# Optimization experiments

Measured on AMD Instinct MI355X. Metric: run time of the kernel, lower is better.

Reference implementation:

```python
import jax, jax.numpy as jnp
import numpy as np

N = 50000
E = 800000
H, C = 8, 16          # heads, per-head channels (H*C = 128)
G = 64                # number of graphs
EPS = 1e-5


def setup_inputs() -> dict:
    key = jax.random.key(0)
    ks = jax.random.split(key, 8)
    x = jax.random.normal(ks[0], (N, 128), dtype=jnp.float32)
    edge_index = jax.random.randint(ks[1], (2, E), 0, N, dtype=jnp.int64)
    batch = jnp.sort(jax.random.randint(ks[2], (N,), 0, G, dtype=jnp.int64))
    W = jax.random.normal(ks[3], (3, 128, 128), dtype=jnp.float32) * 0.08
    att_src = jax.random.normal(ks[4], (3, H, C), dtype=jnp.float32) * 0.1
    att_dst = jax.random.normal(ks[5], (3, H, C), dtype=jnp.float32) * 0.1
    bias = jnp.zeros((3, 128), dtype=jnp.float32)
    gamma = jnp.ones((3, 128), dtype=jnp.float32)
    beta = jnp.zeros((3, 128), dtype=jnp.float32)
    ro_w = jax.random.normal(ks[6], (128, 2), dtype=jnp.float32) * 0.08
    ro_b = jnp.zeros((2,), dtype=jnp.float32)
    return {"x": x, "edge_index": edge_index, "batch": batch, "W": W,
            "att_src": att_src, "att_dst": att_dst, "bias": bias,
            "gamma": gamma, "beta": beta, "ro_w": ro_w, "ro_b": ro_b}


def _gat_block(prev, h, src, dst, W, a_s, a_d, b, g, be):
    # GATConv (concat=True, add_self_loops already applied to src/dst)
    xp = (h @ W).reshape(N, H, C)                       # [N,H,C]
    al_s = jnp.sum(xp * a_s, axis=-1)                   # [N,H]
    al_d = jnp.sum(xp * a_d, axis=-1)                   # [N,H]
    logits = jax.nn.leaky_relu(al_s[src] + al_d[dst], negative_slope=0.2)  # [Et,H]
    m = jax.ops.segment_max(logits, dst, num_segments=N)        # softmax over dst groups
    ex = jnp.exp(logits - m[dst])
    denom = jax.ops.segment_sum(ex, dst, num_segments=N)
    alpha = ex / denom[dst]                              # [Et,H]
    msg = xp[src] * alpha[:, :, None]                    # [Et,H,C]
    agg = jax.ops.segment_sum(msg, dst, num_segments=N).reshape(N, H * C) + b
    y = prev + agg
    # BatchNorm1d (training mode: batch stats, biased variance)
    mu = y.mean(axis=0)
    var = y.var(axis=0)
    yn = (y - mu) / jnp.sqrt(var + EPS) * g + be
    return jax.nn.elu(yn)


def reference(x, edge_index, batch, W, att_src, att_dst, bias, gamma, beta, ro_w, ro_b):
    loops = jnp.arange(N, dtype=edge_index.dtype)
    src = jnp.concatenate([edge_index[0], loops])        # PyG add_self_loops=True
    dst = jnp.concatenate([edge_index[1], loops])
    h = x
    prev = jnp.zeros((N, 128), dtype=x.dtype)
    for i in range(3):
        out = _gat_block(prev, h, src, dst, W[i], att_src[i], att_dst[i],
                         bias[i], gamma[i], beta[i])
        prev = h[:, :128]
        h = out
    # global mean pool over graphs
    sums = jax.ops.segment_sum(h, batch, num_segments=G)
    cnt = jax.ops.segment_sum(jnp.ones((N,), dtype=h.dtype), batch, num_segments=G)
    pooled = sums / jnp.maximum(cnt, 1.0)[:, None]
    return pooled @ ro_w + ro_b
```

## Files before the change

### kernel.cpp

```cpp
#include <hip/hip_runtime.h>
#include <hip/hip_bf16.h>
#include <math.h>

#define NN 50000
#define EE 800000
#define MM (EE + NN)
#define GG 64
#define SWG 512
#define NSB ((NN + 255) / 256)
#define PSP 16

__device__ __forceinline__ int geti(const void* p, long idx, int is64) {
    return is64 ? (int)((const long long*)p)[idx] : ((const int*)p)[idx];
}

__device__ __forceinline__ float bf2f(unsigned short u) {
    return __uint_as_float(((unsigned)u) << 16);
}

__device__ __forceinline__ float eluf(float z) {
    return z > 0.f ? z : expm1f(z);
}

__global__ void k_detect(const int* __restrict__ ei, int* __restrict__ flag) {
    if (blockIdx.x == 0 && threadIdx.x == 0) {
        int ok = 1;
        for (int k = 0; k < 128; ++k) {
            int lo = ei[2 * k], hi = ei[2 * k + 1];
            if (hi != 0 || (unsigned)lo >= (unsigned)NN) { ok = 0; break; }
        }
        flag[0] = ok;
    }
}


__global__ void k_zero(int* p, int n) {
    int i = blockIdx.x * blockDim.x + threadIdx.x;
    if (i < n) p[i] = 0;
}

__global__ void k_count(const void* __restrict__ ei, const int* __restrict__ flag,
                        int* __restrict__ counts) {
    int e = blockIdx.x * blockDim.x + threadIdx.x;
    if (e >= MM) return;
    int is64 = flag[0];
    int d = (e < EE) ? geti(ei, (long)EE + e, is64) : (e - EE);
    if ((unsigned)d < (unsigned)NN) atomicAdd(&counts[d], 1);
}

__global__ __launch_bounds__(256) void k_scan1(const int* __restrict__ counts,
                                               int* __restrict__ rowptr,
                                               int* __restrict__ bsum) {
    __shared__ int buf[256];
    int b = blockIdx.x, tid = threadIdx.x;
    int i = b * 256 + tid;
    int v = (i < NN) ? counts[i] : 0;
    buf[tid] = v;
    __syncthreads();
    for (int off = 1; off < 256; off <<= 1) {
        int t = (tid >= off) ? buf[tid - off] : 0;
        __syncthreads();
        buf[tid] += t;
        __syncthreads();
    }
    if (i < NN) rowptr[i + 1] = buf[tid];
    if (tid == 255) bsum[b] = buf[255];
}

__global__ __launch_bounds__(256) void k_scan2(int* __restrict__ bsum) {
    __shared__ int buf[256];
    int tid = threadIdx.x;
    int v = (tid < NSB) ? bsum[tid] : 0;
    buf[tid] = v;
    __syncthreads();
    for (int off = 1; off < 256; off <<= 1) {
        int t = (tid >= off) ? buf[tid - off] : 0;
        __syncthreads();
        buf[tid] += t;
        __syncthreads();
    }
    if (tid < NSB) bsum[tid] = (tid == 0) ? 0 : buf[tid - 1];
}

__global__ __launch_bounds__(256) void k_scan3(int* __restrict__ rowptr,
                                               const int* __restrict__ bsum) {
    int b = blockIdx.x, tid = threadIdx.x;
    int i = b * 256 + tid;
    if (i < NN) rowptr[i + 1] += bsum[b];
    if (b == 0 && tid == 0) rowptr[0] = 0;
}

__global__ void k_fill(const void* __restrict__ ei, const int* __restrict__ flag,
                       const int* __restrict__ rowptr,
                       int* __restrict__ fill, int* __restrict__ colv) {
    int e = blockIdx.x * blockDim.x + threadIdx.x;
    if (e >= MM) return;
    int is64 = flag[0];
    int s, d;
    if (e < EE) { s = geti(ei, e, is64); d = geti(ei, (long)EE + e, is64); }
    else { s = d = e - EE; }
    if ((unsigned)d >= (unsigned)NN || (unsigned)s >= (unsigned)NN) return;
    int pos = rowptr[d] + atomicAdd(&fill[d], 1);
    if ((unsigned)pos < (unsigned)MM) colv[pos] = s;
}


__global__ __launch_bounds__(256) void k_gemm_att(
    const float* __restrict__ hsrc, const float* __restrict__ Ysrc,
    const float* __restrict__ st, const float* __restrict__ W,
    const float* __restrict__ attS, const float* __restrict__ attD,
    unsigned short* __restrict__ xpb, float* __restrict__ als,
    float* __restrict__ ald, int n)
{
    __shared__ float Wt[32][128];
    __shared__ float Ht[128][33];
    int tid = threadIdx.x;
    int head = tid & 7, r0 = tid >> 3;
    int rbase = blockIdx.x * 128;
    bool useY = (Ysrc != nullptr);

    float acc[4][16];
#pragma unroll
    for (int a = 0; a < 4; ++a)
#pragma unroll
        for (int b = 0; b < 16; ++b) acc[a][b] = 0.f;

    for (int k0 = 0; k0 < 128; k0 += 32) {
#pragma unroll
        for (int j = 0; j < 4; ++j) {
            int idx = tid * 16 + j * 4;
            int kk = idx >> 7, c = idx & 127;
            *(float4*)&Wt[kk][c] = *(const float4*)&W[(k0 + kk) * 128 + c];
        }
#pragma unroll
        for (int j = 0; j < 4; ++j) {
            int f = tid * 16 + j * 4;
            int r = f >> 5, kk = f & 31;
            int gr = rbase + r;
            float4 v = make_float4(0.f, 0.f, 0.f, 0.f);
            if (gr < n) {
                if (useY) {
                    float4 yv = *(const float4*)&Ysrc[gr * 128 + k0 + kk];
                    float4 scv = *(const float4*)&st[k0 + kk];
                    float4 shv = *(const float4*)&st[128 + k0 + kk];
                    v.x = eluf(fmaf(yv.x, scv.x, shv.x));
                    v.y = eluf(fmaf(yv.y, scv.y, shv.y));
                    v.z = eluf(fmaf(yv.z, scv.z, shv.z));
                    v.w = eluf(fmaf(yv.w, scv.w, shv.w));
                } else {
                    v = *(const float4*)&hsrc[gr * 128 + k0 + kk];
                }
            }
            Ht[r][kk] = v.x; Ht[r][kk + 1] = v.y; Ht[r][kk + 2] = v.z; Ht[r][kk + 3] = v.w;
        }
        __syncthreads();
#pragma unroll
        for (int kk = 0; kk < 32; ++kk) {
            float wv[16];
#pragma unroll
            for (int j = 0; j < 4; ++j)
                *(float4*)&wv[j * 4] = *(const float4*)&Wt[kk][head * 16 + j * 4];
#pragma unroll
            for (int rr = 0; rr < 4; ++rr) {
                float hv = Ht[r0 + rr * 32][kk];
#pragma unroll
                for (int j = 0; j < 16; ++j) acc[rr][j] = fmaf(hv, wv[j], acc[rr][j]);
            }
        }
        __syncthreads();
    }

    float asv[16], adv[16];
#pragma unroll
    for (int j = 0; j < 16; ++j) { asv[j] = attS[head * 16 + j]; adv[j] = attD[head * 16 + j]; }

#pragma unroll
    for (int rr = 0; rr < 4; ++rr) {
        int r = rbase + r0 + rr * 32;
        if (r < n) {
            float ds = 0.f, dd = 0.f;
#pragma unroll
            for (int j = 0; j < 16; ++j) { ds = fmaf(acc[rr][j], asv[j], ds); dd = fmaf(acc[rr][j], adv[j], dd); }
            als[r * 8 + head] = ds;
            ald[r * 8 + head] = dd;
            unsigned short xb[16];
#pragma unroll
            for (int j = 0; j < 16; ++j) {
                __hip_bfloat16 t = __float2bfloat16(acc[rr][j]);
                xb[j] = *reinterpret_cast<unsigned short*>(&t);
            }
            *(uint4*)&xpb[r * 128 + head * 16]     = *(uint4*)&xb[0];
            *(uint4*)&xpb[r * 128 + head * 16 + 8] = *(uint4*)&xb[8];
        }
    }
}


__global__ __launch_bounds__(256) void k_agg(
    const unsigned short* __restrict__ xpb, const float* __restrict__ als,
    const float* __restrict__ ald,
    const int* __restrict__ rowptr, const int* __restrict__ colv,
    const float* __restrict__ prevRaw, const float* __restrict__ prevY,
    const float* __restrict__ pst, const float* __restrict__ bias,
    float* __restrict__ y, int n)
{
    __shared__ float alds[4][8][8];
    __shared__ int   slds[4][8];
    int wv = threadIdx.x >> 6;
    int wid = (int)((blockIdx.x * blockDim.x + threadIdx.x) >> 6);
    int lane = threadIdx.x & 63;
    if (wid >= n) return;
    int rs = rowptr[wid], re = rowptr[wid + 1];
    int deg = re - rs;

    int hd = lane & 7;
    int ee = lane >> 3;
    float aldn = ald[wid * 8 + hd];
    int q = lane >> 3;
    int c0 = lane * 2;

    float a0 = 0.f, a1 = 0.f, smloc = 0.f;
    int full = deg & ~7;

    for (int b0 = 0; b0 < full; b0 += 8) {
        int se = colv[rs + b0 + ee];
        float v = als[se * 8 + hd] + aldn;
        v = v > 0.f ? v : 0.2f * v;
        float al = expf(v);
        smloc += al;
        alds[wv][ee][hd] = al;
        if (hd == 0) slds[wv][ee] = se;
#pragma unroll
        for (int j = 0; j < 8; ++j) {
            int s = slds[wv][j];
            float a = alds[wv][j][q];
            ushort2 xv = *(const ushort2*)(xpb + (size_t)s * 128 + c0);
            a0 = fmaf(a, bf2f(xv.x), a0);
            a1 = fmaf(a, bf2f(xv.y), a1);
        }
    }

    if (full < deg) {
        int nb = deg - full;
        float al = 0.f;
        int se = 0;
        if (ee < nb) {
            se = colv[rs + full + ee];
            float v = als[se * 8 + hd] + aldn;
            v = v > 0.f ? v : 0.2f * v;
            al = expf(v);
            smloc += al;
        }
        alds[wv][ee][hd] = al;
        if (hd == 0) slds[wv][ee] = se;
        for (int j = 0; j < nb; ++j) {
            int s = slds[wv][j];
            float a = alds[wv][j][q];
            ushort2 xv = *(const ushort2*)(xpb + (size_t)s * 128 + c0);
            a0 = fmaf(a, bf2f(xv.x), a0);
            a1 = fmaf(a, bf2f(xv.y), a1);
        }
    }

    smloc += __shfl_xor(smloc, 8);
    smloc += __shfl_xor(smloc, 16);
    smloc += __shfl_xor(smloc, 32);
    float inv = 1.f / __shfl(smloc, q);
    a0 *= inv;
    a1 *= inv;

    float p0 = 0.f, p1 = 0.f;
    if (prevY) {
        float2 yv = *(const float2*)(prevY + (size_t)wid * 128 + c0);
        p0 = eluf(fmaf(yv.x, pst[c0], pst[128 + c0]));
        p1 = eluf(fmaf(yv.y, pst[c0 + 1], pst[129 + c0]));
    } else if (prevRaw) {
        p0 = prevRaw[(size_t)wid * 128 + c0];
        p1 = prevRaw[(size_t)wid * 128 + c0 + 1];
    }
    y[wid * 128 + c0] = p0 + a0 + bias[c0];
    y[wid * 128 + c0 + 1] = p1 + a1 + bias[c0 + 1];
}


__global__ __launch_bounds__(256) void k_stats(const float* __restrict__ y,
                                               double* __restrict__ partial, int n) {
    int col = threadIdx.x & 127;
    int rg = threadIdx.x >> 7;
    double s = 0.0, s2 = 0.0;
    for (int r = blockIdx.x * 2 + rg; r < n; r += SWG * 2) {
        float v = y[r * 128 + col];
        s += v; s2 += (double)v * (double)v;
    }
    __shared__ double ls[256], ls2[256];
    ls[threadIdx.x] = s; ls2[threadIdx.x] = s2;
    __syncthreads();
    if (rg == 0) {
        s += ls[threadIdx.x + 128];
        s2 += ls2[threadIdx.x + 128];
        partial[col * SWG + blockIdx.x] = s;
        partial[128 * SWG + col * SWG + blockIdx.x] = s2;
    }
}

__global__ void k_stats_fin(const double* __restrict__ partial,
                            const float* __restrict__ gamma,
                            const float* __restrict__ beta,
                            float* __restrict__ st, int n) {
    int col = threadIdx.x;
    double s = 0.0, s2 = 0.0;
    for (int w = 0; w < SWG; ++w) {
        s += partial[col * SWG + w];
        s2 += partial[128 * SWG + col * SWG + w];
    }
    double mu = s / n;
    double var = s2 / n - mu * mu;
    double rsig = 1.0 / sqrt(var + 1e-5);
    double sc = (double)gamma[col] * rsig;
    st[col] = (float)sc;
    st[128 + col] = (float)((double)beta[col] - mu * sc);
}


__global__ __launch_bounds__(256) void k_pool_part(
    const float* __restrict__ Y, const float* __restrict__ st,
    const void* __restrict__ batch, const int* __restrict__ flag,
    float* __restrict__ ppart, int n)
{
    int g = blockIdx.x / PSP;
    int sp = blockIdx.x % PSP;
    int is64 = flag[0];
    int lo = 0, hi = n;
    while (lo < hi) { int mid = (lo + hi) >> 1; if (geti(batch, mid, is64) < g) lo = mid + 1; else hi = mid; }
    int start = lo;
    hi = n;
    while (lo < hi) { int mid = (lo + hi) >> 1; if (geti(batch, mid, is64) < g + 1) lo = mid + 1; else hi = mid; }
    int end = lo;
    int cnt = end - start;
    int slice = (cnt + PSP - 1) / PSP;
    int s0 = start + sp * slice;
    int s1 = s0 + slice; if (s1 > end) s1 = end;

    int col = threadIdx.x & 127;
    int half = threadIdx.x >> 7;
    float sc = st[col], sh = st[128 + col];
    float s = 0.f;
    for (int r = s0 + half; r < s1; r += 2)
        s += eluf(fmaf(Y[(size_t)r * 128 + col], sc, sh));
    __shared__ float ls[256];
    ls[threadIdx.x] = s;
    __syncthreads();
    if (half == 0) ppart[(g * PSP + sp) * 128 + col] = s + ls[col + 128];
}

__global__ __launch_bounds__(128) void k_pool_fin(
    const float* __restrict__ ppart, const void* __restrict__ batch,
    const int* __restrict__ flag, const float* __restrict__ row,
    const float* __restrict__ rob, float* __restrict__ out, int n)
{
    int g = blockIdx.x;
    int is64 = flag[0];
    int lo = 0, hi = n;
    while (lo < hi) { int mid = (lo + hi) >> 1; if (geti(batch, mid, is64) < g) lo = mid + 1; else hi = mid; }
    int start = lo;
    hi = n;
    while (lo < hi) { int mid = (lo + hi) >> 1; if (geti(batch, mid, is64) < g + 1) lo = mid + 1; else hi = mid; }
    int cnt = lo - start;

    int col = threadIdx.x;
    float s = 0.f;
#pragma unroll
    for (int sp = 0; sp < PSP; ++sp) s += ppart[(g * PSP + sp) * 128 + col];
    __shared__ float ls[128];
    ls[col] = s * (1.f / fmaxf((float)cnt, 1.f));
    __syncthreads();
    if (col < 2) {
        float acc = 0.f;
        for (int c = 0; c < 128; ++c) acc = fmaf(ls[c], row[c * 2 + col], acc);
        out[g * 2 + col] = acc + rob[col];
    }
}


extern "C" void kernel_launch(void* const* d_in, const int* in_sizes, int n_in,
                              void* d_out, int out_size, void* d_ws, size_t ws_size,
                              hipStream_t stream) {
    const float* x     = (const float*)d_in[0];
    const void*  ei    = d_in[1];
    const void*  batch = d_in[2];
    const float* W     = (const float*)d_in[3];
    const float* attS  = (const float*)d_in[4];
    const float* attD  = (const float*)d_in[5];
    const float* bias  = (const float*)d_in[6];
    const float* gamma = (const float*)d_in[7];
    const float* beta  = (const float*)d_in[8];
    const float* row   = (const float*)d_in[9];
    const float* rob   = (const float*)d_in[10];
    float* out = (float*)d_out;

    char* wsb = (char*)d_ws;
    size_t off = 0;
    auto alloc = [&](size_t bytes) {
        void* p = wsb + off;
        off += (bytes + 255) & ~(size_t)255;
        return p;
    };
    int*    flag    = (int*)alloc(256);
    int*    rowptr  = (int*)alloc((size_t)(NN + 1) * 4);
    int*    cnts    = (int*)alloc((size_t)NN * 4 * 2);
    int*    bsum    = (int*)alloc((size_t)256 * 4);
    int*    colv    = (int*)alloc((size_t)MM * 4);
    double* partial = (double*)alloc((size_t)128 * SWG * 2 * 8);
    float*  st1     = (float*)alloc(256 * 4);
    float*  st2     = (float*)alloc(256 * 4);
    float*  st3     = (float*)alloc(256 * 4);
    float*  ppart   = (float*)alloc((size_t)GG * PSP * 128 * 4);
    float*  ALS     = (float*)alloc((size_t)NN * 8 * 4);
    float*  ALD     = (float*)alloc((size_t)NN * 8 * 4);
    unsigned short* XPB = (unsigned short*)alloc((size_t)NN * 128 * 2);
    float* Y1 = (float*)alloc((size_t)NN * 128 * 4);
    float* Y2 = (float*)alloc((size_t)NN * 128 * 4);
    float* Y3 = (float*)alloc((size_t)NN * 128 * 4);
    (void)ws_size; (void)in_sizes; (void)n_in; (void)out_size;

    int* fill = cnts + NN;
    const int GB = (NN + 127) / 128;
    const int GA = (NN + 3) / 4;

    hipLaunchKernelGGL(k_detect, dim3(1), dim3(64), 0, stream, (const int*)ei, flag);
    hipLaunchKernelGGL(k_zero, dim3((2 * NN + 255) / 256), dim3(256), 0, stream, cnts, 2 * NN);
    hipLaunchKernelGGL(k_count, dim3((MM + 255) / 256), dim3(256), 0, stream, ei, flag, cnts);
    hipLaunchKernelGGL(k_scan1, dim3(NSB), dim3(256), 0, stream, cnts, rowptr, bsum);
    hipLaunchKernelGGL(k_scan2, dim3(1), dim3(256), 0, stream, bsum);
    hipLaunchKernelGGL(k_scan3, dim3(NSB), dim3(256), 0, stream, rowptr, bsum);
    hipLaunchKernelGGL(k_fill, dim3((MM + 255) / 256), dim3(256), 0, stream, ei, flag, rowptr, fill, colv);

    hipLaunchKernelGGL(k_gemm_att, dim3(GB), dim3(256), 0, stream,
                       x, (const float*)nullptr, (const float*)nullptr,
                       W, attS, attD, XPB, ALS, ALD, NN);
    hipLaunchKernelGGL(k_agg, dim3(GA), dim3(256), 0, stream,
                       XPB, ALS, ALD, rowptr, colv,
                       (const float*)nullptr, (const float*)nullptr, (const float*)nullptr,
                       bias, Y1, NN);
    hipLaunchKernelGGL(k_stats, dim3(SWG), dim3(256), 0, stream, Y1, partial, NN);
    hipLaunchKernelGGL(k_stats_fin, dim3(1), dim3(128), 0, stream, partial, gamma, beta, st1, NN);

    hipLaunchKernelGGL(k_gemm_att, dim3(GB), dim3(256), 0, stream,
                       (const float*)nullptr, Y1, st1,
                       W + 16384, attS + 128, attD + 128, XPB, ALS, ALD, NN);
    hipLaunchKernelGGL(k_agg, dim3(GA), dim3(256), 0, stream,
                       XPB, ALS, ALD, rowptr, colv,
                       x, (const float*)nullptr, (const float*)nullptr,
                       bias + 128, Y2, NN);
    hipLaunchKernelGGL(k_stats, dim3(SWG), dim3(256), 0, stream, Y2, partial, NN);
    hipLaunchKernelGGL(k_stats_fin, dim3(1), dim3(128), 0, stream, partial, gamma + 128, beta + 128, st2, NN);

    hipLaunchKernelGGL(k_gemm_att, dim3(GB), dim3(256), 0, stream,
                       (const float*)nullptr, Y2, st2,
                       W + 32768, attS + 256, attD + 256, XPB, ALS, ALD, NN);
    hipLaunchKernelGGL(k_agg, dim3(GA), dim3(256), 0, stream,
                       XPB, ALS, ALD, rowptr, colv,
                       (const float*)nullptr, Y1, st1,
                       bias + 256, Y3, NN);
    hipLaunchKernelGGL(k_stats, dim3(SWG), dim3(256), 0, stream, Y3, partial, NN);
    hipLaunchKernelGGL(k_stats_fin, dim3(1), dim3(128), 0, stream, partial, gamma + 256, beta + 256, st3, NN);

    hipLaunchKernelGGL(k_pool_part, dim3(GG * PSP), dim3(256), 0, stream,
                       Y3, st3, batch, flag, ppart, NN);
    hipLaunchKernelGGL(k_pool_fin, dim3(GG), dim3(128), 0, stream,
                       ppart, batch, flag, row, rob, out, NN);
}
```

Before: 532.0 us.

## Split GEMM+attention kernel into half-column tiles with padded W layout

Each block of the projection kernel now computes only 64 of the 128 output columns, so twice as many blocks are launched and each thread holds 32 accumulators instead of 64. The shared W tile is stored padded per 8-column group to ease bank conflicts, and each head's attention dot product is completed across two lanes with a shuffle. The goal is lower register pressure and higher occupancy. The cost is that every input row tile, including the BN+ELU transform on layers 2 and 3, is loaded and computed twice.

```diff
diff --git a/kernel.cpp b/kernel.cpp
--- a/kernel.cpp
+++ b/kernel.cpp
@@ -112,25 +112,30 @@
     unsigned short* __restrict__ xpb, float* __restrict__ als,
     float* __restrict__ ald, int n)
 {
-    __shared__ float Wt[32][128];
+    __shared__ float Wt[32][8][12];
     __shared__ float Ht[128][33];
     int tid = threadIdx.x;
-    int head = tid & 7, r0 = tid >> 3;
-    int rbase = blockIdx.x * 128;
+    int hh = tid & 7;
+    int r0 = tid >> 3;
+    int rbase = (blockIdx.x >> 1) * 128;
+    int cbase = (blockIdx.x & 1) * 64;
     bool useY = (Ysrc != nullptr);
 
-    float acc[4][16];
+    float acc[4][8];
 #pragma unroll
     for (int a = 0; a < 4; ++a)
 #pragma unroll
-        for (int b = 0; b < 16; ++b) acc[a][b] = 0.f;
+        for (int b = 0; b < 8; ++b) acc[a][b] = 0.f;
 
     for (int k0 = 0; k0 < 128; k0 += 32) {
 #pragma unroll
-        for (int j = 0; j < 4; ++j) {
-            int idx = tid * 16 + j * 4;
-            int kk = idx >> 7, c = idx & 127;
-            *(float4*)&Wt[kk][c] = *(const float4*)&W[(k0 + kk) * 128 + c];
+        for (int jj = 0; jj < 2; ++jj) {
+            int idx = tid * 2 + jj;
+            int kk = idx >> 4;
+            int cpos = (idx & 15) * 4;
+            int h2 = cpos >> 3, t = cpos & 7;
+            *(float4*)&Wt[kk][h2][t] =
+                *(const float4*)&W[(k0 + kk) * 128 + cbase + h2 * 8 + t];
         }
 #pragma unroll
         for (int j = 0; j < 4; ++j) {
@@ -154,25 +159,29 @@
             Ht[r][kk] = v.x; Ht[r][kk + 1] = v.y; Ht[r][kk + 2] = v.z; Ht[r][kk + 3] = v.w;
         }
         __syncthreads();
-#pragma unroll
+#pragma unroll 4
         for (int kk = 0; kk < 32; ++kk) {
-            float wv[16];
-#pragma unroll
-            for (int j = 0; j < 4; ++j)
-                *(float4*)&wv[j * 4] = *(const float4*)&Wt[kk][head * 16 + j * 4];
+            float wv[8];
+            *(float4*)&wv[0] = *(const float4*)&Wt[kk][hh][0];
+            *(float4*)&wv[4] = *(const float4*)&Wt[kk][hh][4];
 #pragma unroll
             for (int rr = 0; rr < 4; ++rr) {
                 float hv = Ht[r0 + rr * 32][kk];
 #pragma unroll
-                for (int j = 0; j < 16; ++j) acc[rr][j] = fmaf(hv, wv[j], acc[rr][j]);
+                for (int j = 0; j < 8; ++j) acc[rr][j] = fmaf(hv, wv[j], acc[rr][j]);
             }
         }
         __syncthreads();
     }
 
-    float asv[16], adv[16];
-#pragma unroll
-    for (int j = 0; j < 16; ++j) { asv[j] = attS[head * 16 + j]; adv[j] = attD[head * 16 + j]; }
+    int head = (cbase >> 4) + (hh >> 1);
+    int halfsel = hh & 1;
+    float asv[8], adv[8];
+#pragma unroll
+    for (int j = 0; j < 8; ++j) {
+        asv[j] = attS[head * 16 + halfsel * 8 + j];
+        adv[j] = attD[head * 16 + halfsel * 8 + j];
+    }
 
 #pragma unroll
     for (int rr = 0; rr < 4; ++rr) {
@@ -180,17 +189,20 @@
         if (r < n) {
             float ds = 0.f, dd = 0.f;
 #pragma unroll
-            for (int j = 0; j < 16; ++j) { ds = fmaf(acc[rr][j], asv[j], ds); dd = fmaf(acc[rr][j], adv[j], dd); }
-            als[r * 8 + head] = ds;
-            ald[r * 8 + head] = dd;
-            unsigned short xb[16];
-#pragma unroll
-            for (int j = 0; j < 16; ++j) {
+            for (int j = 0; j < 8; ++j) { ds = fmaf(acc[rr][j], asv[j], ds); dd = fmaf(acc[rr][j], adv[j], dd); }
+            ds += __shfl_xor(ds, 1);
+            dd += __shfl_xor(dd, 1);
+            if (halfsel == 0) {
+                als[r * 8 + head] = ds;
+                ald[r * 8 + head] = dd;
+            }
+            unsigned short xb[8];
+#pragma unroll
+            for (int j = 0; j < 8; ++j) {
                 __hip_bfloat16 t = __float2bfloat16(acc[rr][j]);
                 xb[j] = *reinterpret_cast<unsigned short*>(&t);
             }
-            *(uint4*)&xpb[r * 128 + head * 16]     = *(uint4*)&xb[0];
-            *(uint4*)&xpb[r * 128 + head * 16 + 8] = *(uint4*)&xb[8];
+            *(uint4*)&xpb[(size_t)r * 128 + cbase + hh * 8] = *(uint4*)&xb[0];
         }
     }
 }
@@ -424,7 +436,7 @@
     (void)ws_size; (void)in_sizes; (void)n_in; (void)out_size;
 
     int* fill = cnts + NN;
-    const int GB = (NN + 127) / 128;
+    const int GB2 = ((NN + 127) / 128) * 2;
     const int GA = (NN + 3) / 4;
 
     hipLaunchKernelGGL(k_detect, dim3(1), dim3(64), 0, stream, (const int*)ei, flag);
@@ -435,7 +447,7 @@
     hipLaunchKernelGGL(k_scan3, dim3(NSB), dim3(256), 0, stream, rowptr, bsum);
     hipLaunchKernelGGL(k_fill, dim3((MM + 255) / 256), dim3(256), 0, stream, ei, flag, rowptr, fill, colv);
 
-    hipLaunchKernelGGL(k_gemm_att, dim3(GB), dim3(256), 0, stream,
+    hipLaunchKernelGGL(k_gemm_att, dim3(GB2), dim3(256), 0, stream,
                        x, (const float*)nullptr, (const float*)nullptr,
                        W, attS, attD, XPB, ALS, ALD, NN);
     hipLaunchKernelGGL(k_agg, dim3(GA), dim3(256), 0, stream,
@@ -445,7 +457,7 @@
     hipLaunchKernelGGL(k_stats, dim3(SWG), dim3(256), 0, stream, Y1, partial, NN);
     hipLaunchKernelGGL(k_stats_fin, dim3(1), dim3(128), 0, stream, partial, gamma, beta, st1, NN);
 
-    hipLaunchKernelGGL(k_gemm_att, dim3(GB), dim3(256), 0, stream,
+    hipLaunchKernelGGL(k_gemm_att, dim3(GB2), dim3(256), 0, stream,
                        (const float*)nullptr, Y1, st1,
                        W + 16384, attS + 128, attD + 128, XPB, ALS, ALD, NN);
     hipLaunchKernelGGL(k_agg, dim3(GA), dim3(256), 0, stream,
@@ -455,7 +467,7 @@
     hipLaunchKernelGGL(k_stats, dim3(SWG), dim3(256), 0, stream, Y2, partial, NN);
     hipLaunchKernelGGL(k_stats_fin, dim3(1), dim3(128), 0, stream, partial, gamma + 128, beta + 128, st2, NN);
 
-    hipLaunchKernelGGL(k_gemm_att, dim3(GB), dim3(256), 0, stream,
+    hipLaunchKernelGGL(k_gemm_att, dim3(GB2), dim3(256), 0, stream,
                        (const float*)nullptr, Y2, st2,
                        W + 32768, attS + 256, attD + 256, XPB, ALS, ALD, NN);
     hipLaunchKernelGGL(k_agg, dim3(GA), dim3(256), 0, stream,
```

Measured after the change: 545.1 us. 1.02x slower.
